# Kernel optimization log

Measured on AMD Instinct MI355X. Metric: run time of the kernel, lower is better.

The kernel has to match this reference:

```python
import jax, jax.numpy as jnp
import numpy as np

N_GENES = 15135
K = int(np.ceil(0.5 * N_GENES))  # 7568, PyG TopKPooling ratio=0.5
BS, E, F_IN, H, HF, NC, L = 8, 242160, 64, 128, 512, 2, 3


def setup_inputs() -> dict:
    key = jax.random.key(0)
    ks = jax.random.split(key, 16)
    def lin(k, fin, fout):
        s = 1.0 / np.sqrt(fin)
        return jax.random.normal(k, (fin, fout), jnp.float32) * s
    x = jax.random.normal(ks[0], (BS, N_GENES, F_IN), jnp.float32)
    batch = jnp.zeros((BS,), jnp.int32)
    edge_index = jax.random.randint(ks[1], (2, E), 0, N_GENES, dtype=jnp.int32)
    CAT = L * H
    return {
        "x": x,
        "batch": batch,
        "edge_index": edge_index,
        "W1": lin(ks[2], F_IN, H), "b1": jnp.zeros((H,), jnp.float32),
        "W2": lin(ks[3], H, H),    "b2": jnp.zeros((H,), jnp.float32),
        "W3": lin(ks[4], H, H),    "b3": jnp.zeros((H,), jnp.float32),
        "topk_w": jax.random.normal(ks[5], (CAT,), jnp.float32) / np.sqrt(CAT),
        "fcW": lin(ks[6], CAT, 1), "fcb": jnp.zeros((1,), jnp.float32),
        "lin1W": lin(ks[7], K, HF), "lin1b": jnp.zeros((HF,), jnp.float32),
        "lin2W": lin(ks[8], HF, NC), "lin2b": jnp.zeros((NC,), jnp.float32),
    }


def reference(x, batch, edge_index, W1, b1, W2, b2, W3, b3,
              topk_w, fcW, fcb, lin1W, lin1b, lin2W, lin2b):
    bs = x.shape[0]
    # --- GCN normalization with self-loops (PyG GCNConv defaults) ---
    loop = jnp.arange(N_GENES, dtype=edge_index.dtype)
    src = jnp.concatenate([edge_index[0], loop])
    dst = jnp.concatenate([edge_index[1], loop])
    deg = jnp.zeros((N_GENES,), x.dtype).at[dst].add(1.0)
    dinv = jax.lax.rsqrt(deg)  # deg >= 1 due to self-loops
    norm = dinv[src] * dinv[dst]  # [E+N]

    def gcn(h, W, b):
        h = h @ W                                   # [bs, N, H]
        msg = h[:, src, :] * norm[None, :, None]    # gather + edge weight
        agg = jnp.zeros_like(h).at[:, dst, :].add(msg)  # scatter-add
        return agg + b

    h1 = jax.nn.relu(gcn(x, W1, b1))
    h2 = jax.nn.relu(gcn(h1, W2, b2))
    h3 = jax.nn.relu(gcn(h2, W3, b3))
    # mode='cat': stack on last dim then flatten -> feature order (H, layer)
    xc = jnp.stack([h1, h2, h3], -1).reshape(bs, N_GENES, -1)  # [bs, N, L*H]

    # --- TopKPooling (score = tanh(x.w/||w||), keep top ceil(0.5*N)) ---
    score = jnp.tanh((xc @ topk_w) / jnp.linalg.norm(topk_w))  # [bs, N]
    top_s, perm = jax.lax.top_k(score, K)                       # [bs, K]
    xp = jnp.take_along_axis(xc, perm[..., None], axis=1) * top_s[..., None]

    z = (xp @ fcW + fcb)[..., 0]          # [bs, K]
    h = jax.nn.relu(z @ lin1W + lin1b)    # [bs, HF]; dropout inactive (eval)
    logits = h @ lin2W + lin2b            # [bs, NC]
    return jax.nn.log_softmax(logits, axis=-1)
```

## Files before the change

### kernel.cpp

```cpp
#include <hip/hip_runtime.h>

#define N_G   15135
#define E_N   242160
#define BSZ   8
#define K_TOP 7568
#define NH    128
#define NBIN  65536
#define SUFS  65600

typedef float f4v __attribute__((ext_vector_type(4)));
typedef float f2v __attribute__((ext_vector_type(2)));

__global__ void zero_kernel(int* __restrict__ p, int n) {
  int i = blockIdx.x * 1024 + threadIdx.x;
  if (i < n) p[i] = 0;
}

__global__ void count_kernel(const int* __restrict__ ei, int* __restrict__ cnt) {
  int e = blockIdx.x * 256 + threadIdx.x;
  if (e < E_N) atomicAdd(&cnt[ei[E_N + e]], 1);
}

__global__ __launch_bounds__(1024) void scan_kernel(const int* __restrict__ cnt,
                                                    int* __restrict__ rowstart,
                                                    float* __restrict__ dinv,
                                                    int4* __restrict__ rowdesc,
                                                    int* __restrict__ gctr,
                                                    const float* __restrict__ topk_w,
                                                    float* __restrict__ scal) {
  __shared__ int buf[1024];
  __shared__ int base;
  int tid = threadIdx.x;
  int i = blockIdx.x * 1024 + tid;
  int v = (i < N_G) ? cnt[i] : 0;
  float di = 1.0f / sqrtf((float)(v + 1));
  if (i < N_G) dinv[i] = di;
  buf[tid] = v;
  __syncthreads();
  for (int s = 1; s < 1024; s <<= 1) {
    int t = (tid >= s) ? buf[tid - s] : 0;
    __syncthreads();
    buf[tid] += t;
    __syncthreads();
  }
  if (tid == 1023) base = atomicAdd(gctr, buf[1023]);
  __syncthreads();
  if (i < N_G) {
    int rs = base + buf[tid] - v;
    rowstart[i] = rs;
    rowdesc[i] = make_int4(rs, v, __float_as_int(di), 0);
  }
  if (blockIdx.x == 0) {
    __shared__ float fbuf[512];
    if (tid < 512) {
      float w = (tid < 384) ? topk_w[tid] : 0.f;
      fbuf[tid] = w * w;
    }
    __syncthreads();
    for (int s = 256; s > 0; s >>= 1) {
      if (tid < s) fbuf[tid] += fbuf[tid + s];
      __syncthreads();
    }
    if (tid == 0) scal[0] = 1.0f / sqrtf(fbuf[0]);
  }
}

__global__ void fill_kernel(const int* __restrict__ ei, const int* __restrict__ rowstart,
                            const float* __restrict__ dinv, int* __restrict__ fillc,
                            int2* __restrict__ csr) {
  int e = blockIdx.x * 256 + threadIdx.x;
  if (e < E_N) {
    int s = ei[e], d = ei[E_N + e];
    int pos = rowstart[d] + atomicAdd(&fillc[d], 1);
    csr[pos] = make_int2(s, __float_as_int(dinv[s]));
  }
}

template<int CIN, bool BR>
__global__ __launch_bounds__(256, 6) void mm_kernel(const float* __restrict__ A,
                                                    const float* __restrict__ W,
                                                    const float* __restrict__ bias,
                                                    float* __restrict__ out) {
  __shared__ float Bst[32][132];
  __shared__ float Ast2[32][68];
  int tid = threadIdx.x;
  int b = blockIdx.x & 7;
  int ib = blockIdx.x >> 3;
  int rb0 = b * N_G + ib * 64;
  int rmax = N_G - ib * 64;
  int c0 = (tid & 31) * 4;
  int r0 = (tid >> 5) * 8;
  float acc[8][4];
#pragma unroll
  for (int i = 0; i < 8; i++)
#pragma unroll
    for (int j = 0; j < 4; j++) acc[i][j] = 0.f;

  for (int k0 = 0; k0 < CIN; k0 += 32) {
    {
      int koff = (tid & 7) * 4;
      int row = tid >> 3;
#pragma unroll
      for (int p = 0; p < 2; ++p) {
        int r = row + p * 32;
        f4v v = {0.f, 0.f, 0.f, 0.f};
        if (r < rmax) v = __builtin_nontemporal_load((const f4v*)(A + (size_t)(rb0 + r) * CIN + k0 + koff));
        Ast2[koff + 0][r] = v.x; Ast2[koff + 1][r] = v.y;
        Ast2[koff + 2][r] = v.z; Ast2[koff + 3][r] = v.w;
      }
    }
    {
      int cc = (tid & 31) * 4;
      int kr = tid >> 5;
#pragma unroll
      for (int p = 0; p < 4; ++p) {
        int k = kr + p * 8;
        *(float4*)&Bst[k][cc] = *(const float4*)(W + (size_t)(k0 + k) * NH + cc);
      }
    }
    __syncthreads();
#pragma unroll 4
    for (int kk = 0; kk < 32; ++kk) {
      float a[8], bb[4];
      *(float4*)&a[0] = *(const float4*)&Ast2[kk][r0];
      *(float4*)&a[4] = *(const float4*)&Ast2[kk][r0 + 4];
      *(float4*)&bb[0] = *(const float4*)&Bst[kk][c0];
#pragma unroll
      for (int i = 0; i < 8; i++)
#pragma unroll
        for (int j = 0; j < 4; j++)
          acc[i][j] = fmaf(a[i], bb[j], acc[i][j]);
    }
    __syncthreads();
  }
  float b0 = 0.f, b1 = 0.f, b2 = 0.f, b3 = 0.f;
  if (BR) { b0 = bias[c0]; b1 = bias[c0+1]; b2 = bias[c0+2]; b3 = bias[c0+3]; }
#pragma unroll
  for (int i = 0; i < 8; i++) {
    int r = r0 + i;
    if (r < rmax) {
      float4 v;
      if (BR) {
        v.x = fmaxf(acc[i][0] + b0, 0.f); v.y = fmaxf(acc[i][1] + b1, 0.f);
        v.z = fmaxf(acc[i][2] + b2, 0.f); v.w = fmaxf(acc[i][3] + b3, 0.f);
      } else {
        v.x = acc[i][0]; v.y = acc[i][1]; v.z = acc[i][2]; v.w = acc[i][3];
      }
      *(float4*)(out + (size_t)(rb0 + r) * NH + c0) = v;
    }
  }
}

__global__ __launch_bounds__(256) void agg64_kernel(const float* __restrict__ src,
                                                    const int2* __restrict__ csr,
                                                    const int4* __restrict__ rowdesc,
                                                    float* __restrict__ dst) {
  int b = blockIdx.x & 7;
  int chunk = blockIdx.x >> 3;
  int wave = threadIdx.x >> 6, lane = threadIdx.x & 63;
  int d = chunk * 4 + wave;
  if (d >= N_G) return;
  d = __builtin_amdgcn_readfirstlane(d);
  int4 rd = rowdesc[d];
  int e0 = rd.x, n = rd.y;
  float dv = __int_as_float(rd.z);
  const float* sb = src + (size_t)b * N_G * 64;
  const int2* ce = csr + e0;
  float acc[8];
  acc[0] = dv * sb[(size_t)d * 64 + lane];
#pragma unroll
  for (int k = 1; k < 8; ++k) acc[k] = 0.f;
  int l = 0;
  if (n >= 8) {
    int2 pA[8]; float vA[8];
#pragma unroll
    for (int k = 0; k < 8; ++k) pA[k] = ce[k];
#pragma unroll
    for (int k = 0; k < 8; ++k) vA[k] = sb[(size_t)pA[k].x * 64 + lane];
    l = 8;
    for (; l + 8 <= n; l += 8) {
      int2 pB[8]; float vB[8];
#pragma unroll
      for (int k = 0; k < 8; ++k) pB[k] = ce[l + k];
#pragma unroll
      for (int k = 0; k < 8; ++k) vB[k] = sb[(size_t)pB[k].x * 64 + lane];
#pragma unroll
      for (int k = 0; k < 8; ++k) acc[k] = fmaf(__int_as_float(pA[k].y), vA[k], acc[k]);
#pragma unroll
      for (int k = 0; k < 8; ++k) { pA[k] = pB[k]; vA[k] = vB[k]; }
    }
#pragma unroll
    for (int k = 0; k < 8; ++k) acc[k] = fmaf(__int_as_float(pA[k].y), vA[k], acc[k]);
  }
  for (; l < n; ++l) {
    int2 p = ce[l];
    acc[0] = fmaf(__int_as_float(p.y), sb[(size_t)p.x * 64 + lane], acc[0]);
  }
  float s = ((acc[0] + acc[1]) + (acc[2] + acc[3])) + ((acc[4] + acc[5]) + (acc[6] + acc[7]));
  __builtin_nontemporal_store(dv * s, &dst[((size_t)b * N_G + d) * 64 + lane]);
}

__global__ __launch_bounds__(256) void agg_f2_kernel(const float* __restrict__ hw,
                                                     const int2* __restrict__ csr,
                                                     const int4* __restrict__ rowdesc,
                                                     const float* __restrict__ bias,
                                                     float* __restrict__ hout) {
  int b = blockIdx.x & 7;
  int chunk = blockIdx.x >> 3;
  int wave = threadIdx.x >> 6, lane = threadIdx.x & 63;
  int d0 = chunk * 8 + wave * 2;
  if (d0 >= N_G) return;
  d0 = __builtin_amdgcn_readfirstlane(d0);
  int d1 = d0 + 1;
  int has1 = (d1 < N_G);
  int dB = has1 ? d1 : d0;
  int4 rdA = rowdesc[d0];
  int4 rdB = rowdesc[dB];
  int nA = rdA.y, nB = has1 ? rdB.y : 0;
  float dvA = __int_as_float(rdA.z);
  float dvB = __int_as_float(rdB.z);
  const f2v* sb = (const f2v*)(hw + (size_t)b * N_G * NH);
  const int2* ceA = csr + rdA.x;
  const int2* ceB = csr + rdB.x;
  f2v selfA = sb[(size_t)d0 * 64 + lane];
  f2v selfB = sb[(size_t)dB * 64 + lane];
  float axA[4], ayA[4], axB[4], ayB[4];
  axA[0] = dvA * selfA.x; ayA[0] = dvA * selfA.y;
  axB[0] = has1 ? dvB * selfB.x : 0.f;
  ayB[0] = has1 ? dvB * selfB.y : 0.f;
#pragma unroll
  for (int k = 1; k < 4; ++k) { axA[k] = 0.f; ayA[k] = 0.f; axB[k] = 0.f; ayB[k] = 0.f; }
  int lA = 0, lB = 0;
  while (lA + 8 <= nA && lB + 8 <= nB) {
    int2 pA[8], pB[8]; f2v vA[8], vB[8];
#pragma unroll
    for (int k = 0; k < 8; ++k) pA[k] = ceA[lA + k];
#pragma unroll
    for (int k = 0; k < 8; ++k) pB[k] = ceB[lB + k];
#pragma unroll
    for (int k = 0; k < 8; ++k) vA[k] = sb[(size_t)pA[k].x * 64 + lane];
#pragma unroll
    for (int k = 0; k < 8; ++k) vB[k] = sb[(size_t)pB[k].x * 64 + lane];
#pragma unroll
    for (int k = 0; k < 8; ++k) {
      float w = __int_as_float(pA[k].y);
      axA[k & 3] = fmaf(w, vA[k].x, axA[k & 3]);
      ayA[k & 3] = fmaf(w, vA[k].y, ayA[k & 3]);
    }
#pragma unroll
    for (int k = 0; k < 8; ++k) {
      float w = __int_as_float(pB[k].y);
      axB[k & 3] = fmaf(w, vB[k].x, axB[k & 3]);
      ayB[k & 3] = fmaf(w, vB[k].y, ayB[k & 3]);
    }
    lA += 8; lB += 8;
  }
  for (; lA + 8 <= nA; lA += 8) {
    int2 pA[8]; f2v vA[8];
#pragma unroll
    for (int k = 0; k < 8; ++k) pA[k] = ceA[lA + k];
#pragma unroll
    for (int k = 0; k < 8; ++k) vA[k] = sb[(size_t)pA[k].x * 64 + lane];
#pragma unroll
    for (int k = 0; k < 8; ++k) {
      float w = __int_as_float(pA[k].y);
      axA[k & 3] = fmaf(w, vA[k].x, axA[k & 3]);
      ayA[k & 3] = fmaf(w, vA[k].y, ayA[k & 3]);
    }
  }
  for (; lB + 8 <= nB; lB += 8) {
    int2 pB[8]; f2v vB[8];
#pragma unroll
    for (int k = 0; k < 8; ++k) pB[k] = ceB[lB + k];
#pragma unroll
    for (int k = 0; k < 8; ++k) vB[k] = sb[(size_t)pB[k].x * 64 + lane];
#pragma unroll
    for (int k = 0; k < 8; ++k) {
      float w = __int_as_float(pB[k].y);
      axB[k & 3] = fmaf(w, vB[k].x, axB[k & 3]);
      ayB[k & 3] = fmaf(w, vB[k].y, ayB[k & 3]);
    }
  }
  for (; lA < nA; ++lA) {
    int2 p = ceA[lA];
    f2v v = sb[(size_t)p.x * 64 + lane];
    float w = __int_as_float(p.y);
    axA[0] = fmaf(w, v.x, axA[0]); ayA[0] = fmaf(w, v.y, ayA[0]);
  }
  for (; lB < nB; ++lB) {
    int2 p = ceB[lB];
    f2v v = sb[(size_t)p.x * 64 + lane];
    float w = __int_as_float(p.y);
    axB[0] = fmaf(w, v.x, axB[0]); ayB[0] = fmaf(w, v.y, ayB[0]);
  }
  const f2v* bb2 = (const f2v*)bias;
  f2v bb = bb2[lane];
  {
    float sx = (axA[0] + axA[1]) + (axA[2] + axA[3]);
    float sy = (ayA[0] + ayA[1]) + (ayA[2] + ayA[3]);
    f2v r;
    r.x = fmaxf(fmaf(dvA, sx, bb.x), 0.f);
    r.y = fmaxf(fmaf(dvA, sy, bb.y), 0.f);
    __builtin_nontemporal_store(r, &((f2v*)hout)[((size_t)b * N_G + d0) * 64 + lane]);
  }
  if (has1) {
    float sx = (axB[0] + axB[1]) + (axB[2] + axB[3]);
    float sy = (ayB[0] + ayB[1]) + (ayB[2] + ayB[3]);
    f2v r;
    r.x = fmaxf(fmaf(dvB, sx, bb.x), 0.f);
    r.y = fmaxf(fmaf(dvB, sy, bb.y), 0.f);
    __builtin_nontemporal_store(r, &((f2v*)hout)[((size_t)b * N_G + d1) * 64 + lane]);
  }
}

__global__ __launch_bounds__(256) void agg_score_f2_kernel(const float* __restrict__ hw,
                                                           const int2* __restrict__ csr,
                                                           const int4* __restrict__ rowdesc,
                                                           const float* __restrict__ bias,
                                                           const float* __restrict__ h1,
                                                           const float* __restrict__ h2,
                                                           const float* __restrict__ topk_w,
                                                           const float* __restrict__ fcW,
                                                           const float* __restrict__ scal,
                                                           float* __restrict__ score,
                                                           float* __restrict__ d2a,
                                                           unsigned* __restrict__ keys,
                                                           int* __restrict__ hist) {
  int b = blockIdx.x & 7;
  int chunk = blockIdx.x >> 3;
  int wave = threadIdx.x >> 6, lane = threadIdx.x & 63;
  int d0 = chunk * 8 + wave * 2;
  if (d0 >= N_G) return;
  d0 = __builtin_amdgcn_readfirstlane(d0);
  int d1 = d0 + 1;
  int has1 = (d1 < N_G);
  int dB = has1 ? d1 : d0;
  int4 rdA = rowdesc[d0];
  int4 rdB = rowdesc[dB];
  int nA = rdA.y, nB = has1 ? rdB.y : 0;
  float dvA = __int_as_float(rdA.z);
  float dvB = __int_as_float(rdB.z);
  const f2v* sb = (const f2v*)(hw + (size_t)b * N_G * NH);
  const int2* ceA = csr + rdA.x;
  const int2* ceB = csr + rdB.x;
  size_t rbA = ((size_t)b * N_G + d0) * 64 + lane;
  size_t rbB = ((size_t)b * N_G + dB) * 64 + lane;
  f2v u1A = __builtin_nontemporal_load(&((const f2v*)h1)[rbA]);
  f2v u2A = __builtin_nontemporal_load(&((const f2v*)h2)[rbA]);
  f2v u1B = __builtin_nontemporal_load(&((const f2v*)h1)[rbB]);
  f2v u2B = __builtin_nontemporal_load(&((const f2v*)h2)[rbB]);
  f2v selfA = sb[(size_t)d0 * 64 + lane];
  f2v selfB = sb[(size_t)dB * 64 + lane];
  float axA[4], ayA[4], axB[4], ayB[4];
  axA[0] = dvA * selfA.x; ayA[0] = dvA * selfA.y;
  axB[0] = has1 ? dvB * selfB.x : 0.f;
  ayB[0] = has1 ? dvB * selfB.y : 0.f;
#pragma unroll
  for (int k = 1; k < 4; ++k) { axA[k] = 0.f; ayA[k] = 0.f; axB[k] = 0.f; ayB[k] = 0.f; }
  int lA = 0, lB = 0;
  while (lA + 8 <= nA && lB + 8 <= nB) {
    int2 pA[8], pB[8]; f2v vA[8], vB[8];
#pragma unroll
    for (int k = 0; k < 8; ++k) pA[k] = ceA[lA + k];
#pragma unroll
    for (int k = 0; k < 8; ++k) pB[k] = ceB[lB + k];
#pragma unroll
    for (int k = 0; k < 8; ++k) vA[k] = sb[(size_t)pA[k].x * 64 + lane];
#pragma unroll
    for (int k = 0; k < 8; ++k) vB[k] = sb[(size_t)pB[k].x * 64 + lane];
#pragma unroll
    for (int k = 0; k < 8; ++k) {
      float w = __int_as_float(pA[k].y);
      axA[k & 3] = fmaf(w, vA[k].x, axA[k & 3]);
      ayA[k & 3] = fmaf(w, vA[k].y, ayA[k & 3]);
    }
#pragma unroll
    for (int k = 0; k < 8; ++k) {
      float w = __int_as_float(pB[k].y);
      axB[k & 3] = fmaf(w, vB[k].x, axB[k & 3]);
      ayB[k & 3] = fmaf(w, vB[k].y, ayB[k & 3]);
    }
    lA += 8; lB += 8;
  }
  for (; lA + 8 <= nA; lA += 8) {
    int2 pA[8]; f2v vA[8];
#pragma unroll
    for (int k = 0; k < 8; ++k) pA[k] = ceA[lA + k];
#pragma unroll
    for (int k = 0; k < 8; ++k) vA[k] = sb[(size_t)pA[k].x * 64 + lane];
#pragma unroll
    for (int k = 0; k < 8; ++k) {
      float w = __int_as_float(pA[k].y);
      axA[k & 3] = fmaf(w, vA[k].x, axA[k & 3]);
      ayA[k & 3] = fmaf(w, vA[k].y, ayA[k & 3]);
    }
  }
  for (; lB + 8 <= nB; lB += 8) {
    int2 pB[8]; f2v vB[8];
#pragma unroll
    for (int k = 0; k < 8; ++k) pB[k] = ceB[lB + k];
#pragma unroll
    for (int k = 0; k < 8; ++k) vB[k] = sb[(size_t)pB[k].x * 64 + lane];
#pragma unroll
    for (int k = 0; k < 8; ++k) {
      float w = __int_as_float(pB[k].y);
      axB[k & 3] = fmaf(w, vB[k].x, axB[k & 3]);
      ayB[k & 3] = fmaf(w, vB[k].y, ayB[k & 3]);
    }
  }
  for (; lA < nA; ++lA) {
    int2 p = ceA[lA];
    f2v v = sb[(size_t)p.x * 64 + lane];
    float w = __int_as_float(p.y);
    axA[0] = fmaf(w, v.x, axA[0]); ayA[0] = fmaf(w, v.y, ayA[0]);
  }
  for (; lB < nB; ++lB) {
    int2 p = ceB[lB];
    f2v v = sb[(size_t)p.x * 64 + lane];
    float w = __int_as_float(p.y);
    axB[0] = fmaf(w, v.x, axB[0]); ayB[0] = fmaf(w, v.y, ayB[0]);
  }
  const f2v* bb2 = (const f2v*)bias;
  f2v bb = bb2[lane];
  float rxA = fmaxf(fmaf(dvA, (axA[0] + axA[1]) + (axA[2] + axA[3]), bb.x), 0.f);
  float ryA = fmaxf(fmaf(dvA, (ayA[0] + ayA[1]) + (ayA[2] + ayA[3]), bb.y), 0.f);
  float rxB = fmaxf(fmaf(dvB, (axB[0] + axB[1]) + (axB[2] + axB[3]), bb.x), 0.f);
  float ryB = fmaxf(fmaf(dvB, (ayB[0] + ayB[1]) + (ayB[2] + ayB[3]), bb.y), 0.f);
  const f2v* tw2 = (const f2v*)topk_w;
  const f2v* fw2 = (const f2v*)fcW;
  f2v ta = tw2[lane * 3 + 0], tb = tw2[lane * 3 + 1], tc = tw2[lane * 3 + 2];
  f2v fa = fw2[lane * 3 + 0], fb = fw2[lane * 3 + 1], fc = fw2[lane * 3 + 2];
  float d1A = u1A.x * ta.x + u2A.x * ta.y + rxA * tb.x
            + u1A.y * tb.y + u2A.y * tc.x + ryA * tc.y;
  float d2A = u1A.x * fa.x + u2A.x * fa.y + rxA * fb.x
            + u1A.y * fb.y + u2A.y * fc.x + ryA * fc.y;
  float d1B = u1B.x * ta.x + u2B.x * ta.y + rxB * tb.x
            + u1B.y * tb.y + u2B.y * tc.x + ryB * tc.y;
  float d2B = u1B.x * fa.x + u2B.x * fa.y + rxB * fb.x
            + u1B.y * fb.y + u2B.y * fc.x + ryB * fc.y;
#pragma unroll
  for (int sh = 32; sh > 0; sh >>= 1) {
    d1A += __shfl_down(d1A, sh);
    d2A += __shfl_down(d2A, sh);
    d1B += __shfl_down(d1B, sh);
    d2B += __shfl_down(d2B, sh);
  }
  if (lane == 0) {
    {
      int gw = b * N_G + d0;
      float sc = tanhf(d1A * scal[0]);
      score[gw] = sc;
      d2a[gw] = d2A;
      unsigned u = __float_as_uint(sc);
      unsigned k32 = (u & 0x80000000u) ? ~u : (u | 0x80000000u);
      keys[gw] = k32;
      atomicAdd(&hist[b * NBIN + (int)(k32 >> 16)], 1);
    }
    if (has1) {
      int gw = b * N_G + d1;
      float sc = tanhf(d1B * scal[0]);
      score[gw] = sc;
      d2a[gw] = d2B;
      unsigned u = __float_as_uint(sc);
      unsigned k32 = (u & 0x80000000u) ? ~u : (u | 0x80000000u);
      keys[gw] = k32;
      atomicAdd(&hist[b * NBIN + (int)(k32 >> 16)], 1);
    }
  }
}

__global__ __launch_bounds__(1024) void suffix_kernel(const int* __restrict__ hist,
                                                      int* __restrict__ suf) {
  __shared__ int buf[1024];
  int b = blockIdx.x;
  const int* hb = hist + b * NBIN;
  int* sb = suf + b * SUFS;
  int t = threadIdx.x;
  int base = t * 64;
  int s = 0;
  for (int k = 0; k < 64; ++k) s += hb[base + k];
  buf[t] = s;
  __syncthreads();
  for (int off = 1; off < 1024; off <<= 1) {
    int v = (t + off < 1024) ? buf[t + off] : 0;
    __syncthreads();
    buf[t] += v;
    __syncthreads();
  }
  int acc = buf[t] - s;
  if (t == 0) sb[NBIN] = 0;
  for (int k = 63; k >= 0; --k) {
    acc += hb[base + k];
    sb[base + k] = acc;
  }
}

__global__ void scatter_kernel(const unsigned* __restrict__ keys, int* __restrict__ hist,
                               const int* __restrict__ suf, int2* __restrict__ bucket) {
  int b = blockIdx.y;
  int i = blockIdx.x * 256 + threadIdx.x;
  if (i >= N_G) return;
  unsigned k = keys[b * N_G + i];
  int bin = (int)(k >> 16);
  int old = atomicSub(&hist[b * NBIN + bin], 1);
  int pos = suf[b * SUFS + bin + 1] + old - 1;
  bucket[b * N_G + pos] = make_int2((int)k, i);
}

__global__ void rank_z_kernel(const unsigned* __restrict__ keys, const int* __restrict__ suf,
                              const int2* __restrict__ bucket, const float* __restrict__ score,
                              const float* __restrict__ d2a, const float* __restrict__ fcb,
                              float* __restrict__ z) {
  int b = blockIdx.y;
  int i = blockIdx.x * 256 + threadIdx.x;
  if (i >= N_G) return;
  int gw = b * N_G + i;
  unsigned k = keys[gw];
  int bin = (int)(k >> 16);
  int lo = suf[b * SUFS + bin + 1];
  int hi = suf[b * SUFS + bin];
  int r = lo;
  const int2* bk = bucket + b * N_G;
  for (int p = lo; p < hi; ++p) {
    int2 e = bk[p];
    unsigned kj = (unsigned)e.x;
    r += (kj > k || (kj == k && e.y < i)) ? 1 : 0;
  }
  if (r < K_TOP) z[b * K_TOP + r] = fmaf(score[gw], d2a[gw], fcb[0]);
}

__global__ __launch_bounds__(256) void lin1_kernel(const float* __restrict__ z,
                                                   const float* __restrict__ W,
                                                   float* __restrict__ hpre) {
  __shared__ float zb[237];
  int b = blockIdx.y, rs = blockIdx.x;
  int r0 = rs * 237;
  int rn = K_TOP - r0; if (rn > 237) rn = 237;
  for (int q = threadIdx.x; q < rn; q += 256) zb[q] = z[b * K_TOP + r0 + q];
  __syncthreads();
  int c = threadIdx.x;
  float a0 = 0.f, a1 = 0.f;
  for (int r = 0; r < rn; ++r) {
    float zz = zb[r];
    const float* wr = W + (size_t)(r0 + r) * 512;
    a0 = fmaf(zz, wr[c], a0);
    a1 = fmaf(zz, wr[c + 256], a1);
  }
  atomicAdd(&hpre[b * 512 + c], a0);
  atomicAdd(&hpre[b * 512 + c + 256], a1);
}

__global__ __launch_bounds__(128) void lin2_kernel(const float* __restrict__ hpre,
                                                   const float* __restrict__ l1b,
                                                   const float* __restrict__ W2,
                                                   const float* __restrict__ l2b,
                                                   float* __restrict__ out) {
  int b = blockIdx.x, tid = threadIdx.x;
  float a0 = 0.f, a1 = 0.f;
  for (int j = tid; j < 512; j += 128) {
    float t = fmaxf(hpre[b * 512 + j] + l1b[j], 0.f);
    a0 = fmaf(t, W2[j * 2 + 0], a0);
    a1 = fmaf(t, W2[j * 2 + 1], a1);
  }
#pragma unroll
  for (int s = 32; s > 0; s >>= 1) {
    a0 += __shfl_down(a0, s);
    a1 += __shfl_down(a1, s);
  }
  __shared__ float red[2][2];
  if ((tid & 63) == 0) { red[tid >> 6][0] = a0; red[tid >> 6][1] = a1; }
  __syncthreads();
  if (tid == 0) {
    float l0 = red[0][0] + red[1][0] + l2b[0];
    float l1 = red[0][1] + red[1][1] + l2b[1];
    float m = fmaxf(l0, l1);
    float lse = m + logf(expf(l0 - m) + expf(l1 - m));
    out[b * 2 + 0] = l0 - lse;
    out[b * 2 + 1] = l1 - lse;
  }
}

extern "C" void kernel_launch(void* const* d_in, const int* in_sizes, int n_in,
                              void* d_out, int out_size, void* d_ws, size_t ws_size,
                              hipStream_t stream) {
  const float* x   = (const float*)d_in[0];
  const int*   ei  = (const int*)d_in[2];
  const float* W1  = (const float*)d_in[3];
  const float* b1  = (const float*)d_in[4];
  const float* W2  = (const float*)d_in[5];
  const float* b2  = (const float*)d_in[6];
  const float* W3  = (const float*)d_in[7];
  const float* b3  = (const float*)d_in[8];
  const float* tkw = (const float*)d_in[9];
  const float* fcW = (const float*)d_in[10];
  const float* fcb = (const float*)d_in[11];
  const float* l1W = (const float*)d_in[12];
  const float* l1b = (const float*)d_in[13];
  const float* l2W = (const float*)d_in[14];
  const float* l2b = (const float*)d_in[15];
  float* out = (float*)d_out;

  char* ws = (char*)d_ws;
  size_t off = 0;
  auto alloc = [&](size_t bytes) {
    char* p = ws + off;
    off += (bytes + 255) & ~(size_t)255;
    return p;
  };
  int*   cnt   = (int*)alloc(15136 * 4);
  int*   fillc = (int*)alloc(15136 * 4);
  int*   gctr  = (int*)alloc(256);
  float* hpre  = (float*)alloc(4096 * 4);
  int*   hist  = (int*)alloc((size_t)BSZ * NBIN * 4);
  int*   rowstart = (int*)alloc(15136 * 4);
  float* dinv  = (float*)alloc(15136 * 4);
  int4*  rowdesc = (int4*)alloc(15136 * 16);
  float* scal  = (float*)alloc(64);
  float* z     = (float*)alloc((size_t)BSZ * K_TOP * 4);
  float* score = (float*)alloc(121088 * 4);
  float* d2a   = (float*)alloc(121088 * 4);
  unsigned* keys = (unsigned*)alloc(121088 * 4);
  int*   suf   = (int*)alloc((size_t)BSZ * SUFS * 4);
  int2*  bucket = (int2*)alloc(121088 * 8);
  int2*  csr   = (int2*)alloc((size_t)E_N * 8);
  float* ax = (float*)alloc((size_t)BSZ * N_G * 64 * 4);
  float* hw = (float*)alloc((size_t)BSZ * N_G * NH * 4);
  float* h1 = (float*)alloc((size_t)BSZ * N_G * NH * 4);
  float* h2 = (float*)alloc((size_t)BSZ * N_G * NH * 4);
  (void)ws_size; (void)in_sizes; (void)n_in; (void)out_size;

  int zero_n = (int)(((char*)rowstart - (char*)cnt) / 4);
  zero_kernel<<<(zero_n + 1023) / 1024, 1024, 0, stream>>>(cnt, zero_n);
  count_kernel<<<(E_N + 255) / 256, 256, 0, stream>>>(ei, cnt);
  scan_kernel<<<(N_G + 1023) / 1024, 1024, 0, stream>>>(cnt, rowstart, dinv, rowdesc, gctr, tkw, scal);
  fill_kernel<<<(E_N + 255) / 256, 256, 0, stream>>>(ei, rowstart, dinv, fillc, csr);

  dim3 mmg(8 * 237);
  int aggblocks  = 8 * ((N_G + 3) / 4);
  int aggblocks2 = 8 * ((N_G + 7) / 8);

  agg64_kernel<<<aggblocks, 256, 0, stream>>>(x, csr, rowdesc, ax);
  mm_kernel<64, true><<<mmg, 256, 0, stream>>>(ax, W1, b1, h1);
  mm_kernel<128, false><<<mmg, 256, 0, stream>>>(h1, W2, nullptr, hw);
  agg_f2_kernel<<<aggblocks2, 256, 0, stream>>>(hw, csr, rowdesc, b2, h2);
  mm_kernel<128, false><<<mmg, 256, 0, stream>>>(h2, W3, nullptr, hw);
  agg_score_f2_kernel<<<aggblocks2, 256, 0, stream>>>(hw, csr, rowdesc, b3, h1, h2,
                                                      tkw, fcW, scal, score, d2a, keys, hist);

  dim3 ng((N_G + 255) / 256, BSZ);
  suffix_kernel<<<BSZ, 1024, 0, stream>>>(hist, suf);
  scatter_kernel<<<ng, 256, 0, stream>>>(keys, hist, suf, bucket);
  rank_z_kernel<<<ng, 256, 0, stream>>>(keys, suf, bucket, score, d2a, fcb, z);

  dim3 l1g(32, BSZ);
  lin1_kernel<<<l1g, 256, 0, stream>>>(z, l1W, hpre);
  lin2_kernel<<<BSZ, 128, 0, stream>>>(hpre, l1b, l2W, l2b, out);
}
```

Baseline: 610.5 us.

## Split 128-channel aggregation into two 64-channel half passes

Each 128-wide GCN aggregation kernel becomes two launches that each gather one 64-channel half of the node features, one float per lane. The aim is a smaller working set per pass so gathered rows stay cache-resident (for example in L2 or the last-level cache) during the random neighbour reads. The score kernel carries partial dot products between the two passes in a float2 buffer aliased onto the bucket array. In exchange, the CSR index stream is read twice, there are extra launches, and each gather is a narrower 4-byte load instead of 8 bytes.

```diff
diff --git a/kernel.cpp b/kernel.cpp
--- a/kernel.cpp
+++ b/kernel.cpp
@@ -200,244 +200,186 @@
   __builtin_nontemporal_store(dv * s, &dst[((size_t)b * N_G + d) * 64 + lane]);
 }
 
-__global__ __launch_bounds__(256) void agg_f2_kernel(const float* __restrict__ hw,
-                                                     const int2* __restrict__ csr,
-                                                     const int4* __restrict__ rowdesc,
-                                                     const float* __restrict__ bias,
-                                                     float* __restrict__ hout) {
+template<int CH0>
+__global__ __launch_bounds__(256) void agg_h_kernel(const float* __restrict__ hw,
+                                                    const int2* __restrict__ csr,
+                                                    const int4* __restrict__ rowdesc,
+                                                    const float* __restrict__ bias,
+                                                    float* __restrict__ hout) {
   int b = blockIdx.x & 7;
   int chunk = blockIdx.x >> 3;
   int wave = threadIdx.x >> 6, lane = threadIdx.x & 63;
   int d0 = chunk * 8 + wave * 2;
   if (d0 >= N_G) return;
   d0 = __builtin_amdgcn_readfirstlane(d0);
-  int d1 = d0 + 1;
-  int has1 = (d1 < N_G);
-  int dB = has1 ? d1 : d0;
+  int d1i = d0 + 1;
+  int has1 = (d1i < N_G);
+  int dB = has1 ? d1i : d0;
   int4 rdA = rowdesc[d0];
   int4 rdB = rowdesc[dB];
   int nA = rdA.y, nB = has1 ? rdB.y : 0;
   float dvA = __int_as_float(rdA.z);
   float dvB = __int_as_float(rdB.z);
-  const f2v* sb = (const f2v*)(hw + (size_t)b * N_G * NH);
+  const float* sb = hw + (size_t)b * N_G * NH + CH0 + lane;
   const int2* ceA = csr + rdA.x;
   const int2* ceB = csr + rdB.x;
-  f2v selfA = sb[(size_t)d0 * 64 + lane];
-  f2v selfB = sb[(size_t)dB * 64 + lane];
-  float axA[4], ayA[4], axB[4], ayB[4];
-  axA[0] = dvA * selfA.x; ayA[0] = dvA * selfA.y;
-  axB[0] = has1 ? dvB * selfB.x : 0.f;
-  ayB[0] = has1 ? dvB * selfB.y : 0.f;
-#pragma unroll
-  for (int k = 1; k < 4; ++k) { axA[k] = 0.f; ayA[k] = 0.f; axB[k] = 0.f; ayB[k] = 0.f; }
+  float axA[4], axB[4];
+  axA[0] = dvA * sb[(size_t)d0 * NH];
+  axB[0] = has1 ? dvB * sb[(size_t)dB * NH] : 0.f;
+#pragma unroll
+  for (int k = 1; k < 4; ++k) { axA[k] = 0.f; axB[k] = 0.f; }
   int lA = 0, lB = 0;
   while (lA + 8 <= nA && lB + 8 <= nB) {
-    int2 pA[8], pB[8]; f2v vA[8], vB[8];
+    int2 pA[8], pB[8]; float vA[8], vB[8];
 #pragma unroll
     for (int k = 0; k < 8; ++k) pA[k] = ceA[lA + k];
 #pragma unroll
     for (int k = 0; k < 8; ++k) pB[k] = ceB[lB + k];
 #pragma unroll
-    for (int k = 0; k < 8; ++k) vA[k] = sb[(size_t)pA[k].x * 64 + lane];
-#pragma unroll
-    for (int k = 0; k < 8; ++k) vB[k] = sb[(size_t)pB[k].x * 64 + lane];
-#pragma unroll
-    for (int k = 0; k < 8; ++k) {
-      float w = __int_as_float(pA[k].y);
-      axA[k & 3] = fmaf(w, vA[k].x, axA[k & 3]);
-      ayA[k & 3] = fmaf(w, vA[k].y, ayA[k & 3]);
-    }
-#pragma unroll
-    for (int k = 0; k < 8; ++k) {
-      float w = __int_as_float(pB[k].y);
-      axB[k & 3] = fmaf(w, vB[k].x, axB[k & 3]);
-      ayB[k & 3] = fmaf(w, vB[k].y, ayB[k & 3]);
-    }
+    for (int k = 0; k < 8; ++k) vA[k] = sb[(size_t)pA[k].x * NH];
+#pragma unroll
+    for (int k = 0; k < 8; ++k) vB[k] = sb[(size_t)pB[k].x * NH];
+#pragma unroll
+    for (int k = 0; k < 8; ++k) axA[k & 3] = fmaf(__int_as_float(pA[k].y), vA[k], axA[k & 3]);
+#pragma unroll
+    for (int k = 0; k < 8; ++k) axB[k & 3] = fmaf(__int_as_float(pB[k].y), vB[k], axB[k & 3]);
     lA += 8; lB += 8;
   }
   for (; lA + 8 <= nA; lA += 8) {
-    int2 pA[8]; f2v vA[8];
+    int2 pA[8]; float vA[8];
 #pragma unroll
     for (int k = 0; k < 8; ++k) pA[k] = ceA[lA + k];
 #pragma unroll
-    for (int k = 0; k < 8; ++k) vA[k] = sb[(size_t)pA[k].x * 64 + lane];
-#pragma unroll
-    for (int k = 0; k < 8; ++k) {
-      float w = __int_as_float(pA[k].y);
-      axA[k & 3] = fmaf(w, vA[k].x, axA[k & 3]);
-      ayA[k & 3] = fmaf(w, vA[k].y, ayA[k & 3]);
-    }
+    for (int k = 0; k < 8; ++k) vA[k] = sb[(size_t)pA[k].x * NH];
+#pragma unroll
+    for (int k = 0; k < 8; ++k) axA[k & 3] = fmaf(__int_as_float(pA[k].y), vA[k], axA[k & 3]);
   }
   for (; lB + 8 <= nB; lB += 8) {
-    int2 pB[8]; f2v vB[8];
+    int2 pB[8]; float vB[8];
 #pragma unroll
     for (int k = 0; k < 8; ++k) pB[k] = ceB[lB + k];
 #pragma unroll
-    for (int k = 0; k < 8; ++k) vB[k] = sb[(size_t)pB[k].x * 64 + lane];
-#pragma unroll
-    for (int k = 0; k < 8; ++k) {
-      float w = __int_as_float(pB[k].y);
-      axB[k & 3] = fmaf(w, vB[k].x, axB[k & 3]);
-      ayB[k & 3] = fmaf(w, vB[k].y, ayB[k & 3]);
-    }
+    for (int k = 0; k < 8; ++k) vB[k] = sb[(size_t)pB[k].x * NH];
+#pragma unroll
+    for (int k = 0; k < 8; ++k) axB[k & 3] = fmaf(__int_as_float(pB[k].y), vB[k], axB[k & 3]);
   }
   for (; lA < nA; ++lA) {
     int2 p = ceA[lA];
-    f2v v = sb[(size_t)p.x * 64 + lane];
-    float w = __int_as_float(p.y);
-    axA[0] = fmaf(w, v.x, axA[0]); ayA[0] = fmaf(w, v.y, ayA[0]);
+    axA[0] = fmaf(__int_as_float(p.y), sb[(size_t)p.x * NH], axA[0]);
   }
   for (; lB < nB; ++lB) {
     int2 p = ceB[lB];
-    f2v v = sb[(size_t)p.x * 64 + lane];
-    float w = __int_as_float(p.y);
-    axB[0] = fmaf(w, v.x, axB[0]); ayB[0] = fmaf(w, v.y, ayB[0]);
-  }
-  const f2v* bb2 = (const f2v*)bias;
-  f2v bb = bb2[lane];
+    axB[0] = fmaf(__int_as_float(p.y), sb[(size_t)p.x * NH], axB[0]);
+  }
+  float bb = bias[CH0 + lane];
   {
-    float sx = (axA[0] + axA[1]) + (axA[2] + axA[3]);
-    float sy = (ayA[0] + ayA[1]) + (ayA[2] + ayA[3]);
-    f2v r;
-    r.x = fmaxf(fmaf(dvA, sx, bb.x), 0.f);
-    r.y = fmaxf(fmaf(dvA, sy, bb.y), 0.f);
-    __builtin_nontemporal_store(r, &((f2v*)hout)[((size_t)b * N_G + d0) * 64 + lane]);
+    float s = (axA[0] + axA[1]) + (axA[2] + axA[3]);
+    __builtin_nontemporal_store(fmaxf(fmaf(dvA, s, bb), 0.f),
+        &hout[((size_t)b * N_G + d0) * NH + CH0 + lane]);
   }
   if (has1) {
-    float sx = (axB[0] + axB[1]) + (axB[2] + axB[3]);
-    float sy = (ayB[0] + ayB[1]) + (ayB[2] + ayB[3]);
-    f2v r;
-    r.x = fmaxf(fmaf(dvB, sx, bb.x), 0.f);
-    r.y = fmaxf(fmaf(dvB, sy, bb.y), 0.f);
-    __builtin_nontemporal_store(r, &((f2v*)hout)[((size_t)b * N_G + d1) * 64 + lane]);
-  }
-}
-
-__global__ __launch_bounds__(256) void agg_score_f2_kernel(const float* __restrict__ hw,
-                                                           const int2* __restrict__ csr,
-                                                           const int4* __restrict__ rowdesc,
-                                                           const float* __restrict__ bias,
-                                                           const float* __restrict__ h1,
-                                                           const float* __restrict__ h2,
-                                                           const float* __restrict__ topk_w,
-                                                           const float* __restrict__ fcW,
-                                                           const float* __restrict__ scal,
-                                                           float* __restrict__ score,
-                                                           float* __restrict__ d2a,
-                                                           unsigned* __restrict__ keys,
-                                                           int* __restrict__ hist) {
+    float s = (axB[0] + axB[1]) + (axB[2] + axB[3]);
+    __builtin_nontemporal_store(fmaxf(fmaf(dvB, s, bb), 0.f),
+        &hout[((size_t)b * N_G + d1i) * NH + CH0 + lane]);
+  }
+}
+
+template<int CH0, bool FINAL>
+__global__ __launch_bounds__(256) void agg_score_h_kernel(const float* __restrict__ hw,
+                                                          const int2* __restrict__ csr,
+                                                          const int4* __restrict__ rowdesc,
+                                                          const float* __restrict__ bias,
+                                                          const float* __restrict__ h1,
+                                                          const float* __restrict__ h2,
+                                                          const float* __restrict__ topk_w,
+                                                          const float* __restrict__ fcW,
+                                                          const float* __restrict__ scal,
+                                                          float* __restrict__ score,
+                                                          float* __restrict__ d2a,
+                                                          unsigned* __restrict__ keys,
+                                                          int* __restrict__ hist,
+                                                          float2* __restrict__ dpart) {
   int b = blockIdx.x & 7;
   int chunk = blockIdx.x >> 3;
   int wave = threadIdx.x >> 6, lane = threadIdx.x & 63;
   int d0 = chunk * 8 + wave * 2;
   if (d0 >= N_G) return;
   d0 = __builtin_amdgcn_readfirstlane(d0);
-  int d1 = d0 + 1;
-  int has1 = (d1 < N_G);
-  int dB = has1 ? d1 : d0;
+  int d1i = d0 + 1;
+  int has1 = (d1i < N_G);
+  int dB = has1 ? d1i : d0;
   int4 rdA = rowdesc[d0];
   int4 rdB = rowdesc[dB];
   int nA = rdA.y, nB = has1 ? rdB.y : 0;
   float dvA = __int_as_float(rdA.z);
   float dvB = __int_as_float(rdB.z);
-  const f2v* sb = (const f2v*)(hw + (size_t)b * N_G * NH);
+  const float* sb = hw + (size_t)b * N_G * NH + CH0 + lane;
   const int2* ceA = csr + rdA.x;
   const int2* ceB = csr + rdB.x;
-  size_t rbA = ((size_t)b * N_G + d0) * 64 + lane;
-  size_t rbB = ((size_t)b * N_G + dB) * 64 + lane;
-  f2v u1A = __builtin_nontemporal_load(&((const f2v*)h1)[rbA]);
-  f2v u2A = __builtin_nontemporal_load(&((const f2v*)h2)[rbA]);
-  f2v u1B = __builtin_nontemporal_load(&((const f2v*)h1)[rbB]);
-  f2v u2B = __builtin_nontemporal_load(&((const f2v*)h2)[rbB]);
-  f2v selfA = sb[(size_t)d0 * 64 + lane];
-  f2v selfB = sb[(size_t)dB * 64 + lane];
-  float axA[4], ayA[4], axB[4], ayB[4];
-  axA[0] = dvA * selfA.x; ayA[0] = dvA * selfA.y;
-  axB[0] = has1 ? dvB * selfB.x : 0.f;
-  ayB[0] = has1 ? dvB * selfB.y : 0.f;
-#pragma unroll
-  for (int k = 1; k < 4; ++k) { axA[k] = 0.f; ayA[k] = 0.f; axB[k] = 0.f; ayB[k] = 0.f; }
+  size_t rbA = ((size_t)b * N_G + d0) * NH + CH0 + lane;
+  size_t rbB = ((size_t)b * N_G + dB) * NH + CH0 + lane;
+  float u1A = __builtin_nontemporal_load(&h1[rbA]);
+  float u2A = __builtin_nontemporal_load(&h2[rbA]);
+  float u1B = __builtin_nontemporal_load(&h1[rbB]);
+  float u2B = __builtin_nontemporal_load(&h2[rbB]);
+  float axA[4], axB[4];
+  axA[0] = dvA * sb[(size_t)d0 * NH];
+  axB[0] = has1 ? dvB * sb[(size_t)dB * NH] : 0.f;
+#pragma unroll
+  for (int k = 1; k < 4; ++k) { axA[k] = 0.f; axB[k] = 0.f; }
   int lA = 0, lB = 0;
   while (lA + 8 <= nA && lB + 8 <= nB) {
-    int2 pA[8], pB[8]; f2v vA[8], vB[8];
+    int2 pA[8], pB[8]; float vA[8], vB[8];
 #pragma unroll
     for (int k = 0; k < 8; ++k) pA[k] = ceA[lA + k];
 #pragma unroll
     for (int k = 0; k < 8; ++k) pB[k] = ceB[lB + k];
 #pragma unroll
-    for (int k = 0; k < 8; ++k) vA[k] = sb[(size_t)pA[k].x * 64 + lane];
-#pragma unroll
-    for (int k = 0; k < 8; ++k) vB[k] = sb[(size_t)pB[k].x * 64 + lane];
-#pragma unroll
-    for (int k = 0; k < 8; ++k) {
-      float w = __int_as_float(pA[k].y);
-      axA[k & 3] = fmaf(w, vA[k].x, axA[k & 3]);
-      ayA[k & 3] = fmaf(w, vA[k].y, ayA[k & 3]);
-    }
-#pragma unroll
-    for (int k = 0; k < 8; ++k) {
-      float w = __int_as_float(pB[k].y);
-      axB[k & 3] = fmaf(w, vB[k].x, axB[k & 3]);
-      ayB[k & 3] = fmaf(w, vB[k].y, ayB[k & 3]);
-    }
+    for (int k = 0; k < 8; ++k) vA[k] = sb[(size_t)pA[k].x * NH];
+#pragma unroll
+    for (int k = 0; k < 8; ++k) vB[k] = sb[(size_t)pB[k].x * NH];
+#pragma unroll
+    for (int k = 0; k < 8; ++k) axA[k & 3] = fmaf(__int_as_float(pA[k].y), vA[k], axA[k & 3]);
+#pragma unroll
+    for (int k = 0; k < 8; ++k) axB[k & 3] = fmaf(__int_as_float(pB[k].y), vB[k], axB[k & 3]);
     lA += 8; lB += 8;
   }
   for (; lA + 8 <= nA; lA += 8) {
-    int2 pA[8]; f2v vA[8];
+    int2 pA[8]; float vA[8];
 #pragma unroll
     for (int k = 0; k < 8; ++k) pA[k] = ceA[lA + k];
 #pragma unroll
-    for (int k = 0; k < 8; ++k) vA[k] = sb[(size_t)pA[k].x * 64 + lane];
-#pragma unroll
-    for (int k = 0; k < 8; ++k) {
-      float w = __int_as_float(pA[k].y);
-      axA[k & 3] = fmaf(w, vA[k].x, axA[k & 3]);
-      ayA[k & 3] = fmaf(w, vA[k].y, ayA[k & 3]);
-    }
+    for (int k = 0; k < 8; ++k) vA[k] = sb[(size_t)pA[k].x * NH];
+#pragma unroll
+    for (int k = 0; k < 8; ++k) axA[k & 3] = fmaf(__int_as_float(pA[k].y), vA[k], axA[k & 3]);
   }
   for (; lB + 8 <= nB; lB += 8) {
-    int2 pB[8]; f2v vB[8];
+    int2 pB[8]; float vB[8];
 #pragma unroll
     for (int k = 0; k < 8; ++k) pB[k] = ceB[lB + k];
 #pragma unroll
-    for (int k = 0; k < 8; ++k) vB[k] = sb[(size_t)pB[k].x * 64 + lane];
-#pragma unroll
-    for (int k = 0; k < 8; ++k) {
-      float w = __int_as_float(pB[k].y);
-      axB[k & 3] = fmaf(w, vB[k].x, axB[k & 3]);
-      ayB[k & 3] = fmaf(w, vB[k].y, ayB[k & 3]);
-    }
+    for (int k = 0; k < 8; ++k) vB[k] = sb[(size_t)pB[k].x * NH];
+#pragma unroll
+    for (int k = 0; k < 8; ++k) axB[k & 3] = fmaf(__int_as_float(pB[k].y), vB[k], axB[k & 3]);
   }
   for (; lA < nA; ++lA) {
     int2 p = ceA[lA];
-    f2v v = sb[(size_t)p.x * 64 + lane];
-    float w = __int_as_float(p.y);
-    axA[0] = fmaf(w, v.x, axA[0]); ayA[0] = fmaf(w, v.y, ayA[0]);
+    axA[0] = fmaf(__int_as_float(p.y), sb[(size_t)p.x * NH], axA[0]);
   }
   for (; lB < nB; ++lB) {
     int2 p = ceB[lB];
-    f2v v = sb[(size_t)p.x * 64 + lane];
-    float w = __int_as_float(p.y);
-    axB[0] = fmaf(w, v.x, axB[0]); ayB[0] = fmaf(w, v.y, ayB[0]);
-  }
-  const f2v* bb2 = (const f2v*)bias;
-  f2v bb = bb2[lane];
-  float rxA = fmaxf(fmaf(dvA, (axA[0] + axA[1]) + (axA[2] + axA[3]), bb.x), 0.f);
-  float ryA = fmaxf(fmaf(dvA, (ayA[0] + ayA[1]) + (ayA[2] + ayA[3]), bb.y), 0.f);
-  float rxB = fmaxf(fmaf(dvB, (axB[0] + axB[1]) + (axB[2] + axB[3]), bb.x), 0.f);
-  float ryB = fmaxf(fmaf(dvB, (ayB[0] + ayB[1]) + (ayB[2] + ayB[3]), bb.y), 0.f);
-  const f2v* tw2 = (const f2v*)topk_w;
-  const f2v* fw2 = (const f2v*)fcW;
-  f2v ta = tw2[lane * 3 + 0], tb = tw2[lane * 3 + 1], tc = tw2[lane * 3 + 2];
-  f2v fa = fw2[lane * 3 + 0], fb = fw2[lane * 3 + 1], fc = fw2[lane * 3 + 2];
-  float d1A = u1A.x * ta.x + u2A.x * ta.y + rxA * tb.x
-            + u1A.y * tb.y + u2A.y * tc.x + ryA * tc.y;
-  float d2A = u1A.x * fa.x + u2A.x * fa.y + rxA * fb.x
-            + u1A.y * fb.y + u2A.y * fc.x + ryA * fc.y;
-  float d1B = u1B.x * ta.x + u2B.x * ta.y + rxB * tb.x
-            + u1B.y * tb.y + u2B.y * tc.x + ryB * tc.y;
-  float d2B = u1B.x * fa.x + u2B.x * fa.y + rxB * fb.x
-            + u1B.y * fb.y + u2B.y * fc.x + ryB * fc.y;
+    axB[0] = fmaf(__int_as_float(p.y), sb[(size_t)p.x * NH], axB[0]);
+  }
+  float bb = bias[CH0 + lane];
+  float rA = fmaxf(fmaf(dvA, (axA[0] + axA[1]) + (axA[2] + axA[3]), bb), 0.f);
+  float rB = fmaxf(fmaf(dvB, (axB[0] + axB[1]) + (axB[2] + axB[3]), bb), 0.f);
+  int ch3 = (CH0 + lane) * 3;
+  float t0 = topk_w[ch3 + 0], t1 = topk_w[ch3 + 1], t2 = topk_w[ch3 + 2];
+  float f0 = fcW[ch3 + 0],  f1 = fcW[ch3 + 1],  f2 = fcW[ch3 + 2];
+  float d1A = u1A * t0 + u2A * t1 + rA * t2;
+  float d2A = u1A * f0 + u2A * f1 + rA * f2;
+  float d1B = u1B * t0 + u2B * t1 + rB * t2;
+  float d2B = u1B * f0 + u2B * f1 + rB * f2;
 #pragma unroll
   for (int sh = 32; sh > 0; sh >>= 1) {
     d1A += __shfl_down(d1A, sh);
@@ -446,25 +388,35 @@
     d2B += __shfl_down(d2B, sh);
   }
   if (lane == 0) {
-    {
-      int gw = b * N_G + d0;
-      float sc = tanhf(d1A * scal[0]);
-      score[gw] = sc;
-      d2a[gw] = d2A;
-      unsigned u = __float_as_uint(sc);
-      unsigned k32 = (u & 0x80000000u) ? ~u : (u | 0x80000000u);
-      keys[gw] = k32;
-      atomicAdd(&hist[b * NBIN + (int)(k32 >> 16)], 1);
-    }
-    if (has1) {
-      int gw = b * N_G + d1;
-      float sc = tanhf(d1B * scal[0]);
-      score[gw] = sc;
-      d2a[gw] = d2B;
-      unsigned u = __float_as_uint(sc);
-      unsigned k32 = (u & 0x80000000u) ? ~u : (u | 0x80000000u);
-      keys[gw] = k32;
-      atomicAdd(&hist[b * NBIN + (int)(k32 >> 16)], 1);
+    int gwA = b * N_G + d0;
+    if (!FINAL) {
+      dpart[gwA] = make_float2(d1A, d2A);
+      if (has1) dpart[gwA + 1] = make_float2(d1B, d2B);
+    } else {
+      float sc0 = scal[0];
+      {
+        float2 pp = dpart[gwA];
+        float D1 = pp.x + d1A, D2 = pp.y + d2A;
+        float sc = tanhf(D1 * sc0);
+        score[gwA] = sc;
+        d2a[gwA] = D2;
+        unsigned u = __float_as_uint(sc);
+        unsigned k32 = (u & 0x80000000u) ? ~u : (u | 0x80000000u);
+        keys[gwA] = k32;
+        atomicAdd(&hist[b * NBIN + (int)(k32 >> 16)], 1);
+      }
+      if (has1) {
+        int gwB = gwA + 1;
+        float2 pp = dpart[gwB];
+        float D1 = pp.x + d1B, D2 = pp.y + d2B;
+        float sc = tanhf(D1 * sc0);
+        score[gwB] = sc;
+        d2a[gwB] = D2;
+        unsigned u = __float_as_uint(sc);
+        unsigned k32 = (u & 0x80000000u) ? ~u : (u | 0x80000000u);
+        keys[gwB] = k32;
+        atomicAdd(&hist[b * NBIN + (int)(k32 >> 16)], 1);
+      }
     }
   }
 }
@@ -629,6 +581,8 @@
   float* h2 = (float*)alloc((size_t)BSZ * N_G * NH * 4);
   (void)ws_size; (void)in_sizes; (void)n_in; (void)out_size;
 
+  float2* dpart = (float2*)bucket;
+
   int zero_n = (int)(((char*)rowstart - (char*)cnt) / 4);
   zero_kernel<<<(zero_n + 1023) / 1024, 1024, 0, stream>>>(cnt, zero_n);
   count_kernel<<<(E_N + 255) / 256, 256, 0, stream>>>(ei, cnt);
@@ -642,10 +596,15 @@
   agg64_kernel<<<aggblocks, 256, 0, stream>>>(x, csr, rowdesc, ax);
   mm_kernel<64, true><<<mmg, 256, 0, stream>>>(ax, W1, b1, h1);
   mm_kernel<128, false><<<mmg, 256, 0, stream>>>(h1, W2, nullptr, hw);
-  agg_f2_kernel<<<aggblocks2, 256, 0, stream>>>(hw, csr, rowdesc, b2, h2);
+  agg_h_kernel<0><<<aggblocks2, 256, 0, stream>>>(hw, csr, rowdesc, b2, h2);
+  agg_h_kernel<64><<<aggblocks2, 256, 0, stream>>>(hw, csr, rowdesc, b2, h2);
   mm_kernel<128, false><<<mmg, 256, 0, stream>>>(h2, W3, nullptr, hw);
-  agg_score_f2_kernel<<<aggblocks2, 256, 0, stream>>>(hw, csr, rowdesc, b3, h1, h2,
-                                                      tkw, fcW, scal, score, d2a, keys, hist);
+  agg_score_h_kernel<0, false><<<aggblocks2, 256, 0, stream>>>(hw, csr, rowdesc, b3, h1, h2,
+                                                               tkw, fcW, scal, score, d2a,
+                                                               keys, hist, dpart);
+  agg_score_h_kernel<64, true><<<aggblocks2, 256, 0, stream>>>(hw, csr, rowdesc, b3, h1, h2,
+                                                               tkw, fcW, scal, score, d2a,
+                                                               keys, hist, dpart);
 
   dim3 ng((N_G + 255) / 256, BSZ);
   suffix_kernel<<<BSZ, 1024, 0, stream>>>(hist, suf);
```

New measurement: 638.7 us. +4.6%, slower.
